# Kernel optimization log

Hardware: AMD Instinct MI355X
Metric: run time of the kernel (lower is better)

## Reference

```python
import jax, jax.numpy as jnp
import numpy as np

B, S, F, H = 8, 2048, 512, 4
W = 32            # local window size
DH = F // H       # head dim
EPS = 1e-5


def layer_norm(x, w, b):
    mu = jnp.mean(x, axis=-1, keepdims=True)
    var = jnp.var(x, axis=-1, keepdims=True)
    return (x - mu) * jax.lax.rsqrt(var + EPS) * w + b


def mha(x, w_in, b_in, w_out, b_out):
    # x: [..., L, F]; torch nn.MultiheadAttention self-attention (dropout inactive / eval)
    qkv = x @ w_in.T + b_in                      # [..., L, 3F]
    q, k, v = jnp.split(qkv, 3, axis=-1)
    lead = x.shape[:-2]
    L = x.shape[-2]

    def heads(t):  # [..., L, F] -> [..., H, L, DH]
        return jnp.swapaxes(t.reshape(*lead, L, H, DH), -3, -2)

    q, k, v = heads(q), heads(k), heads(v)
    scores = jnp.einsum('...hld,...hmd->...hlm', q, k) / np.sqrt(DH)
    p = jax.nn.softmax(scores, axis=-1)
    o = jnp.einsum('...hlm,...hmd->...hld', p, v)  # [..., H, L, DH]
    o = jnp.swapaxes(o, -3, -2).reshape(*lead, L, F)
    return o @ w_out.T + b_out


def setup_inputs() -> dict:
    key = jax.random.key(0)
    ks = jax.random.split(key, 16)
    s = 0.02
    p = lambda k, shape: jax.random.normal(k, shape, dtype=jnp.float32) * s
    return {
        'x': jax.random.normal(ks[0], (B, S, F), dtype=jnp.float32),
        'l_in_w': p(ks[1], (3 * F, F)), 'l_in_b': p(ks[2], (3 * F,)),
        'l_out_w': p(ks[3], (F, F)),   'l_out_b': p(ks[4], (F,)),
        'g_in_w': p(ks[5], (3 * F, F)), 'g_in_b': p(ks[6], (3 * F,)),
        'g_out_w': p(ks[7], (F, F)),   'g_out_b': p(ks[8], (F,)),
        'n1_w': jnp.ones((F,)), 'n1_b': jnp.zeros((F,)),
        'n2_w': jnp.ones((F,)), 'n2_b': jnp.zeros((F,)),
        'gate_w': p(ks[9], (F, 2 * F)), 'gate_b': p(ks[10], (F,)),
        'gln_w': jnp.ones((F,)), 'gln_b': jnp.zeros((F,)),
    }


def reference(x, l_in_w, l_in_b, l_out_w, l_out_b,
              g_in_w, g_in_b, g_out_w, g_out_b,
              n1_w, n1_b, n2_w, n2_b,
              gate_w, gate_b, gln_w, gln_b):
    # local branch: block-diagonal (windowed) self-attention, all windows batched
    xw = x.reshape(B, S // W, W, F)
    local = mha(xw, l_in_w, l_in_b, l_out_w, l_out_b).reshape(B, S, F)
    local = layer_norm(x + local, n1_w, n1_b)
    # global branch: full self-attention
    glob = mha(x, g_in_w, g_in_b, g_out_w, g_out_b)
    glob = layer_norm(x + glob, n2_w, n2_b)
    # learned gate fusion
    gi = jnp.concatenate([local, glob], axis=-1)
    gate = jax.nn.sigmoid(layer_norm(gi @ gate_w.T + gate_b, gln_w, gln_b))
    return gate * local + (1.0 - gate) * glob
```

## Files before the change

### kernel.cpp

```cpp
#include <hip/hip_runtime.h>
#include <stdint.h>

#define BB 8
#define SS 2048
#define FF 512
#define HH 4
#define TOK (BB * SS)

typedef unsigned short u16;
typedef short short8 __attribute__((ext_vector_type(8)));
typedef float f32x4 __attribute__((ext_vector_type(4)));
typedef float f32x16 __attribute__((ext_vector_type(16)));
typedef unsigned int u32x4 __attribute__((ext_vector_type(4)));

static __device__ __forceinline__ u16 f2bf(float f) {
  uint32_t u = __builtin_bit_cast(uint32_t, f);
  u = (u + 0x7fffu + ((u >> 16) & 1u)) >> 16;
  return (u16)u;
}

static __device__ __forceinline__ uint32_t cvtpk(float lo, float hi) {
  uint32_t r;
  asm("v_cvt_pk_bf16_f32 %0, %1, %2" : "=v"(r) : "v"(lo), "v"(hi));
  return r;
}

static __device__ __forceinline__ void cp16(void* lds, const void* g) {
  __builtin_amdgcn_global_load_lds(
      (const __attribute__((address_space(1))) void*)g,
      (__attribute__((address_space(3))) void*)lds, 16, 0, 0);
}

__global__ __launch_bounds__(256) void castk(const float* __restrict__ s,
                                             u16* __restrict__ d, int n) {
  const int i = (blockIdx.x * 256 + threadIdx.x) * 8;
  if (i >= n) return;
  float4 a = *(const float4*)(s + i);
  float4 b = *(const float4*)(s + i + 4);
  short8 o;
  o[0] = (short)f2bf(a.x); o[1] = (short)f2bf(a.y);
  o[2] = (short)f2bf(a.z); o[3] = (short)f2bf(a.w);
  o[4] = (short)f2bf(b.x); o[5] = (short)f2bf(b.y);
  o[6] = (short)f2bf(b.z); o[7] = (short)f2bf(b.w);
  *(short8*)(d + i) = o;
}

__global__ __launch_bounds__(256) void gemm_bt(
    const u16* __restrict__ A, const u16* __restrict__ B,
    const float* __restrict__ bias, float* __restrict__ Cf,
    u16* __restrict__ Cb, int M, int N, int K, int qcols, float qscale) {
  const int m0 = blockIdx.x << 7;
  const int n0 = blockIdx.y << 7;
  __shared__ u16 As[128 * 64];
  __shared__ u16 Bs[128 * 64];
  const int tid = threadIdx.x;
  const int wave = tid >> 6, lane = tid & 63;
  const int wr = wave >> 1, wc = wave & 1;

  f32x4 acc[4][4];
#pragma unroll
  for (int i = 0; i < 4; ++i)
#pragma unroll
    for (int j = 0; j < 4; ++j)
#pragma unroll
      for (int e = 0; e < 4; ++e) acc[i][j][e] = 0.f;

  for (int k0 = 0; k0 < K; k0 += 64) {
#pragma unroll
    for (int i = 0; i < 4; ++i) {
      const int base = (i * 4 + wave) << 10;
      const int lb = base + (lane << 4);
      const int r = lb >> 7;
      const int s = ((lb >> 4) & 7) ^ (r & 7);
      cp16((char*)As + base, A + (size_t)(m0 + r) * K + k0 + s * 8);
      cp16((char*)Bs + base, B + (size_t)(n0 + r) * K + k0 + s * 8);
    }
    __syncthreads();
#pragma unroll
    for (int kk = 0; kk < 2; ++kk) {
      short8 af[4], bfr[4];
#pragma unroll
      for (int mi = 0; mi < 4; ++mi) {
        const int r = wr * 64 + mi * 16 + (lane & 15);
        const int p = (kk * 4 + (lane >> 4)) ^ (r & 7);
        af[mi] = *(const short8*)(As + r * 64 + p * 8);
      }
#pragma unroll
      for (int ni = 0; ni < 4; ++ni) {
        const int r = wc * 64 + ni * 16 + (lane & 15);
        const int p = (kk * 4 + (lane >> 4)) ^ (r & 7);
        bfr[ni] = *(const short8*)(Bs + r * 64 + p * 8);
      }
#pragma unroll
      for (int mi = 0; mi < 4; ++mi)
#pragma unroll
        for (int ni = 0; ni < 4; ++ni)
          acc[mi][ni] = __builtin_amdgcn_mfma_f32_16x16x32_bf16(
              af[mi], bfr[ni], acc[mi][ni], 0, 0, 0);
    }
    __syncthreads();
  }
  const int rv = (lane >> 4) << 2;
  const int cn = lane & 15;
#pragma unroll
  for (int mi = 0; mi < 4; ++mi)
#pragma unroll
    for (int ni = 0; ni < 4; ++ni) {
      const int gn = n0 + wc * 64 + ni * 16 + cn;
      const float bv = bias ? bias[gn] : 0.f;
      const float sc = (gn < qcols) ? qscale : 1.f;
#pragma unroll
      for (int v = 0; v < 4; ++v) {
        const int gm = m0 + wr * 64 + mi * 16 + rv + v;
        const size_t off = (size_t)gm * N + gn;
        const float val = (acc[mi][ni][v] + bv) * sc;
        if (Cf) Cf[off] = val;
        if (Cb) Cb[off] = f2bf(val);
      }
    }
}

__global__ __launch_bounds__(256) void transpose_v(
    const u16* __restrict__ qkv, u16* __restrict__ vt) {
  const int bh = blockIdx.x, st = blockIdx.y, dt = blockIdx.z;
  const int b = bh >> 2, h = bh & 3;
  __shared__ u16 t[64][72];
  const int r = threadIdx.x >> 3;
  const int c8 = (threadIdx.x & 7) * 8;
#pragma unroll
  for (int ph = 0; ph < 2; ++ph) {
    const int srow = ph * 32 + r;
    const u16* src = qkv + (size_t)(b * SS + st * 64 + srow) * 1536 + 1024 +
                     h * 128 + dt * 64 + c8;
    *(short8*)&t[srow][c8] = *(const short8*)src;
  }
  __syncthreads();
#pragma unroll
  for (int ph = 0; ph < 2; ++ph) {
    const int drow = ph * 32 + r;
    short8 o;
#pragma unroll
    for (int j = 0; j < 8; ++j) o[j] = (short)t[c8 + j][drow];
    *(short8*)(vt + ((size_t)bh * 128 + dt * 64 + drow) * SS + st * 64 + c8) = o;
  }
}

template <typename GET>
static __device__ __forceinline__ short8 make_pa(int ks, GET get) {
  const int c0 = (2 * ks) & 3;
  u32x4 pw;
#pragma unroll
  for (int t = 0; t < 2; ++t) {
    uint32_t a = cvtpk(get(4 * c0 + 2 * t), get(4 * c0 + 2 * t + 1));
    uint32_t b = cvtpk(get(4 * (c0 + 1) + 2 * t), get(4 * (c0 + 1) + 2 * t + 1));
    auto r = __builtin_amdgcn_permlane32_swap(a, b, false, false);
    pw[t] = r[0];
    pw[2 + t] = r[1];
  }
  return __builtin_bit_cast(short8, pw);
}

__global__ __launch_bounds__(256) void attn_local(
    const u16* __restrict__ qkv, const u16* __restrict__ vt,
    u16* __restrict__ ao) {
  const int wave = threadIdx.x >> 6, lane = threadIdx.x & 63;
  const int u = blockIdx.x * 4 + wave;
  const int b = u >> 8, w = (u >> 2) & 63, h = u & 3;
  const int q = lane & 31, half = lane >> 5;

  const size_t qbase = (size_t)(b * SS + w * 32 + q) * 1536 + h * 128;
  short8 qf[8];
#pragma unroll
  for (int d8 = 0; d8 < 8; ++d8)
    qf[d8] = *(const short8*)(qkv + qbase + d8 * 16 + half * 8);

  f32x16 s;
#pragma unroll
  for (int e = 0; e < 16; ++e) s[e] = 0.f;
  const size_t kbase = qbase + 512;
#pragma unroll
  for (int d8 = 0; d8 < 8; ++d8) {
    short8 kf = *(const short8*)(qkv + kbase + d8 * 16 + half * 8);
    s = __builtin_amdgcn_mfma_f32_32x32x16_bf16(kf, qf[d8], s, 0, 0, 0);
  }
  float m = s[0];
#pragma unroll
  for (int e = 1; e < 16; ++e) m = fmaxf(m, s[e]);
  m = fmaxf(m, __shfl_xor(m, 32));
  float l = 0.f;
#pragma unroll
  for (int e = 0; e < 16; ++e) { s[e] = exp2f(s[e] - m); l += s[e]; }
  l += __shfl_xor(l, 32);

  f32x16 o[4];
#pragma unroll
  for (int nt = 0; nt < 4; ++nt)
#pragma unroll
    for (int e = 0; e < 16; ++e) o[nt][e] = 0.f;
  const size_t vbase = ((size_t)(b * 4 + h) * 128) * SS + w * 32;
#pragma unroll
  for (int ks = 0; ks < 2; ++ks) {
    short8 pa = make_pa(ks, [&](int e) { return s[e]; });
#pragma unroll
    for (int nt = 0; nt < 4; ++nt) {
      short8 vb = *(const short8*)(vt + vbase + (size_t)(nt * 32 + q) * SS +
                                   ks * 16 + half * 8);
      o[nt] = __builtin_amdgcn_mfma_f32_32x32x16_bf16(pa, vb, o[nt], 0, 0, 0);
    }
  }
  const float rl = 1.f / l;
  const size_t ob = (size_t)(b * SS + w * 32) * FF + h * 128;
#pragma unroll
  for (int e = 0; e < 16; ++e) {
    const int qr = (e & 3) + 8 * (e >> 2) + 4 * half;
    const float rf = __shfl(rl, qr);
#pragma unroll
    for (int nt = 0; nt < 4; ++nt)
      ao[ob + (size_t)qr * FF + nt * 32 + q] = f2bf(o[nt][e] * rf);
  }
}

__global__ __launch_bounds__(256) void attn_global(
    const u16* __restrict__ qkv, const u16* __restrict__ vt,
    u16* __restrict__ ao) {
  const int lb = (blockIdx.x & 7) * 64 + (blockIdx.x >> 3);
  const int bh = lb >> 4, qt = lb & 15;
  const int b = bh >> 2, h = bh & 3;
  const int wave = threadIdx.x >> 6, lane = threadIdx.x & 63;
  const int q = lane & 31, half = lane >> 5;

  __shared__ u16 Ks[2][64 * 128];
  __shared__ u16 Vs[2][128 * 64];

  short8 qf[8];
  const size_t qb = (size_t)(b * SS + qt * 128 + wave * 32 + q) * 1536 + h * 128;
#pragma unroll
  for (int d8 = 0; d8 < 8; ++d8)
    qf[d8] = *(const short8*)(qkv + qb + d8 * 16 + half * 8);

  f32x16 o[4];
#pragma unroll
  for (int nt = 0; nt < 4; ++nt)
#pragma unroll
    for (int e = 0; e < 16; ++e) o[nt][e] = 0.f;
  float m = -3e38f, lsum = 0.f;

  const size_t kbase = (size_t)b * SS * 1536 + 512 + h * 128;
  const size_t vbase = (size_t)bh * 128 * SS;

  auto STAGE = [&](int kt, int bsel) {
    u16* kd = Ks[bsel];
    u16* vd = Vs[bsel];
#pragma unroll
    for (int i = 0; i < 4; ++i) {
      const int base = (i * 4 + wave) << 10;
      const int lbk = base + (lane << 4);
      {
        const int r = lbk >> 8;
        const int sl = ((lbk >> 4) & 15) ^ (r & 7);
        cp16((char*)kd + base,
             qkv + kbase + (size_t)(kt * 64 + r) * 1536 + sl * 8);
      }
      {
        const int d = lbk >> 7;
        const int sl = ((lbk >> 4) & 7) ^ (d & 7);
        cp16((char*)vd + base, vt + vbase + (size_t)d * SS + kt * 64 + sl * 8);
      }
    }
  };
  STAGE(0, 0);
  __syncthreads();
  for (int kt = 0; kt < 32; ++kt) {
    const int cur = kt & 1;
    if (kt + 1 < 32) STAGE(kt + 1, cur ^ 1);
    const u16* Kb = Ks[cur];
    const u16* Vb = Vs[cur];

    f32x16 sa[2];
#pragma unroll
    for (int mt = 0; mt < 2; ++mt)
#pragma unroll
      for (int e = 0; e < 16; ++e) sa[mt][e] = 0.f;
#pragma unroll
    for (int mt = 0; mt < 2; ++mt) {
      const int kr = mt * 32 + q;
#pragma unroll
      for (int d8 = 0; d8 < 8; ++d8) {
        const int ps = (d8 * 2 + half) ^ (kr & 7);
        short8 kf = *(const short8*)(Kb + kr * 128 + ps * 8);
        sa[mt] = __builtin_amdgcn_mfma_f32_32x32x16_bf16(kf, qf[d8], sa[mt], 0, 0, 0);
      }
    }
    float pmax = sa[0][0];
#pragma unroll
    for (int e = 1; e < 16; ++e) pmax = fmaxf(pmax, sa[0][e]);
#pragma unroll
    for (int e = 0; e < 16; ++e) pmax = fmaxf(pmax, sa[1][e]);
    pmax = fmaxf(pmax, __shfl_xor(pmax, 32));
    if (__any(pmax > m + 8.f)) {
      const float mn = fmaxf(m, pmax);
      const float corr = exp2f(m - mn);
      m = mn;
      lsum *= corr;
#pragma unroll
      for (int e = 0; e < 16; ++e) {
        const float cf = __shfl(corr, (e & 3) + 8 * (e >> 2) + 4 * half);
#pragma unroll
        for (int nt = 0; nt < 4; ++nt) o[nt][e] *= cf;
      }
    }
    float la = 0.f;
#pragma unroll
    for (int mt = 0; mt < 2; ++mt)
#pragma unroll
      for (int e = 0; e < 16; ++e) {
        sa[mt][e] = exp2f(sa[mt][e] - m);
        la += sa[mt][e];
      }
    la += __shfl_xor(la, 32);
    lsum += la;
#pragma unroll
    for (int ks = 0; ks < 4; ++ks) {
      const int mt = ks >> 1;
      short8 pa = make_pa(ks, [&](int e) { return sa[mt][e]; });
#pragma unroll
      for (int nt = 0; nt < 4; ++nt) {
        const int d = nt * 32 + q;
        const int ps = (ks * 2 + half) ^ (d & 7);
        short8 vb = *(const short8*)(Vb + d * 64 + ps * 8);
        o[nt] = __builtin_amdgcn_mfma_f32_32x32x16_bf16(pa, vb, o[nt], 0, 0, 0);
      }
    }
    __syncthreads();
  }
  const float rl = 1.f / lsum;
  const size_t ob = (size_t)(b * SS + qt * 128 + wave * 32) * FF + h * 128;
#pragma unroll
  for (int e = 0; e < 16; ++e) {
    const int qr = (e & 3) + 8 * (e >> 2) + 4 * half;
    const float rf = __shfl(rl, qr);
#pragma unroll
    for (int nt = 0; nt < 4; ++nt)
      ao[ob + (size_t)qr * FF + nt * 32 + q] = f2bf(o[nt][e] * rf);
  }
}

__global__ __launch_bounds__(256) void resid_ln(
    float* __restrict__ y, const float* __restrict__ x,
    const float* __restrict__ w, const float* __restrict__ bv_,
    u16* __restrict__ lg) {
  const int wave = threadIdx.x >> 6, lane = threadIdx.x & 63;
  const size_t row = (size_t)blockIdx.x * 4 + wave;
  const int c = lane * 8;
  float* yr = y + row * FF;
  const float* xr = x + row * FF;
  float v[8];
  {
    float4 a0 = *(const float4*)(yr + c), a1 = *(const float4*)(yr + c + 4);
    float4 b0 = *(const float4*)(xr + c), b1 = *(const float4*)(xr + c + 4);
    v[0] = a0.x + b0.x; v[1] = a0.y + b0.y; v[2] = a0.z + b0.z; v[3] = a0.w + b0.w;
    v[4] = a1.x + b1.x; v[5] = a1.y + b1.y; v[6] = a1.z + b1.z; v[7] = a1.w + b1.w;
  }
  float s = 0.f, s2 = 0.f;
#pragma unroll
  for (int e = 0; e < 8; ++e) { s += v[e]; s2 += v[e] * v[e]; }
#pragma unroll
  for (int off = 1; off < 64; off <<= 1) {
    s += __shfl_xor(s, off);
    s2 += __shfl_xor(s2, off);
  }
  const float mu = s * (1.f / 512.f);
  const float var = s2 * (1.f / 512.f) - mu * mu;
  const float rs = rsqrtf(var + 1e-5f);
  float4 w0 = *(const float4*)(w + c), w1 = *(const float4*)(w + c + 4);
  float4 b0 = *(const float4*)(bv_ + c), b1 = *(const float4*)(bv_ + c + 4);
  const float wv[8] = {w0.x, w0.y, w0.z, w0.w, w1.x, w1.y, w1.z, w1.w};
  const float bb[8] = {b0.x, b0.y, b0.z, b0.w, b1.x, b1.y, b1.z, b1.w};
  short8 ob;
#pragma unroll
  for (int e = 0; e < 8; ++e) {
    v[e] = (v[e] - mu) * rs * wv[e] + bb[e];
    ob[e] = (short)f2bf(v[e]);
  }
  *(float4*)(yr + c) = make_float4(v[0], v[1], v[2], v[3]);
  *(float4*)(yr + c + 4) = make_float4(v[4], v[5], v[6], v[7]);
  *(short8*)(lg + row * 1024 + c) = ob;
}

__global__ __launch_bounds__(256) void gate_final(
    const float* __restrict__ gp, const float* __restrict__ loc,
    const float* __restrict__ glo, const float* __restrict__ w,
    const float* __restrict__ bv_, float* __restrict__ out) {
  const int wave = threadIdx.x >> 6, lane = threadIdx.x & 63;
  const size_t row = (size_t)blockIdx.x * 4 + wave;
  const int c = lane * 8;
  const float* gr = gp + row * FF;
  float v[8];
  {
    float4 a0 = *(const float4*)(gr + c), a1 = *(const float4*)(gr + c + 4);
    v[0] = a0.x; v[1] = a0.y; v[2] = a0.z; v[3] = a0.w;
    v[4] = a1.x; v[5] = a1.y; v[6] = a1.z; v[7] = a1.w;
  }
  float s = 0.f, s2 = 0.f;
#pragma unroll
  for (int e = 0; e < 8; ++e) { s += v[e]; s2 += v[e] * v[e]; }
#pragma unroll
  for (int off = 1; off < 64; off <<= 1) {
    s += __shfl_xor(s, off);
    s2 += __shfl_xor(s2, off);
  }
  const float mu = s * (1.f / 512.f);
  const float var = s2 * (1.f / 512.f) - mu * mu;
  const float rs = rsqrtf(var + 1e-5f);
  float4 w0 = *(const float4*)(w + c), w1 = *(const float4*)(w + c + 4);
  float4 b0 = *(const float4*)(bv_ + c), b1 = *(const float4*)(bv_ + c + 4);
  const float wv[8] = {w0.x, w0.y, w0.z, w0.w, w1.x, w1.y, w1.z, w1.w};
  const float bb[8] = {b0.x, b0.y, b0.z, b0.w, b1.x, b1.y, b1.z, b1.w};
  float4 l0 = *(const float4*)(loc + row * FF + c), l1 = *(const float4*)(loc + row * FF + c + 4);
  float4 g0 = *(const float4*)(glo + row * FF + c), g1 = *(const float4*)(glo + row * FF + c + 4);
  const float lv[8] = {l0.x, l0.y, l0.z, l0.w, l1.x, l1.y, l1.z, l1.w};
  const float gv[8] = {g0.x, g0.y, g0.z, g0.w, g1.x, g1.y, g1.z, g1.w};
  float r[8];
#pragma unroll
  for (int e = 0; e < 8; ++e) {
    const float z = (v[e] - mu) * rs * wv[e] + bb[e];
    const float gt = 1.f / (1.f + exp2f(-1.44269504f * z));
    r[e] = gt * lv[e] + (1.f - gt) * gv[e];
  }
  *(float4*)(out + row * FF + c) = make_float4(r[0], r[1], r[2], r[3]);
  *(float4*)(out + row * FF + c + 4) = make_float4(r[4], r[5], r[6], r[7]);
}

extern "C" void kernel_launch(void* const* d_in, const int* in_sizes, int n_in,
                              void* d_out, int out_size, void* d_ws,
                              size_t ws_size, hipStream_t stream) {
  const float* x       = (const float*)d_in[0];
  const float* l_in_w  = (const float*)d_in[1];
  const float* l_in_b  = (const float*)d_in[2];
  const float* l_out_w = (const float*)d_in[3];
  const float* l_out_b = (const float*)d_in[4];
  const float* g_in_w  = (const float*)d_in[5];
  const float* g_in_b  = (const float*)d_in[6];
  const float* g_out_w = (const float*)d_in[7];
  const float* g_out_b = (const float*)d_in[8];
  const float* n1_w    = (const float*)d_in[9];
  const float* n1_b    = (const float*)d_in[10];
  const float* n2_w    = (const float*)d_in[11];
  const float* n2_b    = (const float*)d_in[12];
  const float* gate_w  = (const float*)d_in[13];
  const float* gate_b  = (const float*)d_in[14];
  const float* gln_w   = (const float*)d_in[15];
  const float* gln_b   = (const float*)d_in[16];
  float* out = (float*)d_out;

  const float c1 = 0.12752724808f;

  char* ws = (char*)d_ws;
  u16* x_bf  = (u16*)(ws);
  u16* w_liw = (u16*)(ws + 16777216);
  u16* w_giw = (u16*)(ws + 18350080);
  u16* w_low = (u16*)(ws + 19922944);
  u16* w_gow = (u16*)(ws + 20447232);
  u16* w_gt  = (u16*)(ws + 20971520);
  u16* qkv   = (u16*)(ws + 22020096);
  u16* vt    = (u16*)(ws + 72351744);
  u16* ato   = (u16*)(ws + 89128960);
  float* locf = (float*)(ws + 105906176);
  float* glof = (float*)(ws + 139460608);
  u16* lgbf  = (u16*)(ws + 173015040);
  float* gpre = (float*)(ws + 22020096);

  castk<<<4096, 256, 0, stream>>>(x, x_bf, 8388608);
  castk<<<384, 256, 0, stream>>>(l_in_w, w_liw, 786432);
  castk<<<384, 256, 0, stream>>>(g_in_w, w_giw, 786432);
  castk<<<128, 256, 0, stream>>>(l_out_w, w_low, 262144);
  castk<<<128, 256, 0, stream>>>(g_out_w, w_gow, 262144);
  castk<<<256, 256, 0, stream>>>(gate_w, w_gt, 524288);

  gemm_bt<<<dim3(128, 12), 256, 0, stream>>>(x_bf, w_liw, l_in_b, nullptr, qkv,
                                             TOK, 1536, 512, 512, c1);
  transpose_v<<<dim3(32, 32, 2), 256, 0, stream>>>(qkv, vt);
  attn_local<<<512, 256, 0, stream>>>(qkv, vt, ato);
  gemm_bt<<<dim3(128, 4), 256, 0, stream>>>(ato, w_low, l_out_b, locf, nullptr,
                                            TOK, 512, 512, 0, 1.f);
  resid_ln<<<4096, 256, 0, stream>>>(locf, x, n1_w, n1_b, lgbf);

  gemm_bt<<<dim3(128, 12), 256, 0, stream>>>(x_bf, w_giw, g_in_b, nullptr, qkv,
                                             TOK, 1536, 512, 512, c1);
  transpose_v<<<dim3(32, 32, 2), 256, 0, stream>>>(qkv, vt);
  attn_global<<<512, 256, 0, stream>>>(qkv, vt, ato);
  gemm_bt<<<dim3(128, 4), 256, 0, stream>>>(ato, w_gow, g_out_b, glof, nullptr,
                                            TOK, 512, 512, 0, 1.f);
  resid_ln<<<4096, 256, 0, stream>>>(glof, x, n2_w, n2_b, lgbf + 512);

  gemm_bt<<<dim3(128, 4), 256, 0, stream>>>(lgbf, w_gt, gate_b, gpre, nullptr,
                                            TOK, 512, 1024, 0, 1.f);
  gate_final<<<4096, 256, 0, stream>>>(gpre, locf, glof, gln_w, gln_b, out);
}
```

Baseline: 471.6 us.

## Load K/V fragments directly from global memory in global attention, dropping LDS staging

The global attention kernel no longer double-buffers K and V tiles through shared memory with async copies and barriers. Each wave now reads its K and V MFMA operands straight from global memory (relying on L1/L2 caching) through running pointers, and the launch bounds ask for two blocks per CU. The row max and row sum reductions become tree reductions to shorten dependency chains. This removes LDS traffic and per-tile barriers, but every wave in a block now fetches the same K/V data separately and exposes global load latency without explicit prefetch.

```diff
diff --git a/kernel.cpp b/kernel.cpp
--- a/kernel.cpp
+++ b/kernel.cpp
@@ -220,8 +220,8 @@
   }
 }
 
-__global__ __launch_bounds__(256) void attn_global(
-    const u16* __restrict__ qkv, const u16* __restrict__ vt,
+__global__ __launch_bounds__(256, 2) void attn_global(
+    const u16* __restrict__ qkv, const u16* __restrict__ vtp,
     u16* __restrict__ ao) {
   const int lb = (blockIdx.x & 7) * 64 + (blockIdx.x >> 3);
   const int bh = lb >> 4, qt = lb & 15;
@@ -229,9 +229,6 @@
   const int wave = threadIdx.x >> 6, lane = threadIdx.x & 63;
   const int q = lane & 31, half = lane >> 5;
 
-  __shared__ u16 Ks[2][64 * 128];
-  __shared__ u16 Vs[2][128 * 64];
-
   short8 qf[8];
   const size_t qb = (size_t)(b * SS + qt * 128 + wave * 32 + q) * 1536 + h * 128;
 #pragma unroll
@@ -245,58 +242,40 @@
     for (int e = 0; e < 16; ++e) o[nt][e] = 0.f;
   float m = -3e38f, lsum = 0.f;
 
-  const size_t kbase = (size_t)b * SS * 1536 + 512 + h * 128;
-  const size_t vbase = (size_t)bh * 128 * SS;
-
-  auto STAGE = [&](int kt, int bsel) {
-    u16* kd = Ks[bsel];
-    u16* vd = Vs[bsel];
-#pragma unroll
-    for (int i = 0; i < 4; ++i) {
-      const int base = (i * 4 + wave) << 10;
-      const int lbk = base + (lane << 4);
-      {
-        const int r = lbk >> 8;
-        const int sl = ((lbk >> 4) & 15) ^ (r & 7);
-        cp16((char*)kd + base,
-             qkv + kbase + (size_t)(kt * 64 + r) * 1536 + sl * 8);
-      }
-      {
-        const int d = lbk >> 7;
-        const int sl = ((lbk >> 4) & 7) ^ (d & 7);
-        cp16((char*)vd + base, vt + vbase + (size_t)d * SS + kt * 64 + sl * 8);
-      }
-    }
-  };
-  STAGE(0, 0);
-  __syncthreads();
+  const u16* pk0 = qkv + (size_t)b * SS * 1536 + 512 + (size_t)h * 128 +
+                   (size_t)q * 1536 + half * 8;
+  const u16* pk1 = pk0 + (size_t)32 * 1536;
+  const u16* pvb = vtp + (size_t)bh * 128 * SS + (size_t)q * SS + half * 8;
+  const u16* pv0 = pvb;
+  const u16* pv1 = pvb + (size_t)32 * SS;
+  const u16* pv2 = pvb + (size_t)64 * SS;
+  const u16* pv3 = pvb + (size_t)96 * SS;
+
   for (int kt = 0; kt < 32; ++kt) {
-    const int cur = kt & 1;
-    if (kt + 1 < 32) STAGE(kt + 1, cur ^ 1);
-    const u16* Kb = Ks[cur];
-    const u16* Vb = Vs[cur];
-
     f32x16 sa[2];
 #pragma unroll
     for (int mt = 0; mt < 2; ++mt)
 #pragma unroll
       for (int e = 0; e < 16; ++e) sa[mt][e] = 0.f;
 #pragma unroll
-    for (int mt = 0; mt < 2; ++mt) {
-      const int kr = mt * 32 + q;
-#pragma unroll
-      for (int d8 = 0; d8 < 8; ++d8) {
-        const int ps = (d8 * 2 + half) ^ (kr & 7);
-        short8 kf = *(const short8*)(Kb + kr * 128 + ps * 8);
-        sa[mt] = __builtin_amdgcn_mfma_f32_32x32x16_bf16(kf, qf[d8], sa[mt], 0, 0, 0);
-      }
-    }
-    float pmax = sa[0][0];
-#pragma unroll
-    for (int e = 1; e < 16; ++e) pmax = fmaxf(pmax, sa[0][e]);
-#pragma unroll
-    for (int e = 0; e < 16; ++e) pmax = fmaxf(pmax, sa[1][e]);
-    pmax = fmaxf(pmax, __shfl_xor(pmax, 32));
+    for (int d8 = 0; d8 < 8; ++d8) {
+      short8 kf0 = *(const short8*)(pk0 + d8 * 16);
+      sa[0] = __builtin_amdgcn_mfma_f32_32x32x16_bf16(kf0, qf[d8], sa[0], 0, 0, 0);
+    }
+#pragma unroll
+    for (int d8 = 0; d8 < 8; ++d8) {
+      short8 kf1 = *(const short8*)(pk1 + d8 * 16);
+      sa[1] = __builtin_amdgcn_mfma_f32_32x32x16_bf16(kf1, qf[d8], sa[1], 0, 0, 0);
+    }
+    float t[16];
+#pragma unroll
+    for (int e = 0; e < 16; ++e) t[e] = fmaxf(sa[0][e], sa[1][e]);
+#pragma unroll
+    for (int st = 8; st >= 1; st >>= 1)
+#pragma unroll
+      for (int e = 0; e < 8; ++e)
+        if (e < st) t[e] = fmaxf(t[e], t[e + st]);
+    float pmax = fmaxf(t[0], __shfl_xor(t[0], 32));
     if (__any(pmax > m + 8.f)) {
       const float mn = fmaxf(m, pmax);
       const float corr = exp2f(m - mn);
@@ -309,29 +288,35 @@
         for (int nt = 0; nt < 4; ++nt) o[nt][e] *= cf;
       }
     }
-    float la = 0.f;
 #pragma unroll
     for (int mt = 0; mt < 2; ++mt)
 #pragma unroll
-      for (int e = 0; e < 16; ++e) {
-        sa[mt][e] = exp2f(sa[mt][e] - m);
-        la += sa[mt][e];
-      }
-    la += __shfl_xor(la, 32);
-    lsum += la;
+      for (int e = 0; e < 16; ++e) sa[mt][e] = exp2f(sa[mt][e] - m);
+    float u[16];
+#pragma unroll
+    for (int e = 0; e < 16; ++e) u[e] = sa[0][e] + sa[1][e];
+#pragma unroll
+    for (int st = 8; st >= 1; st >>= 1)
+#pragma unroll
+      for (int e = 0; e < 8; ++e)
+        if (e < st) u[e] += u[e + st];
+    lsum += u[0] + __shfl_xor(u[0], 32);
 #pragma unroll
     for (int ks = 0; ks < 4; ++ks) {
       const int mt = ks >> 1;
       short8 pa = make_pa(ks, [&](int e) { return sa[mt][e]; });
-#pragma unroll
-      for (int nt = 0; nt < 4; ++nt) {
-        const int d = nt * 32 + q;
-        const int ps = (ks * 2 + half) ^ (d & 7);
-        short8 vb = *(const short8*)(Vb + d * 64 + ps * 8);
-        o[nt] = __builtin_amdgcn_mfma_f32_32x32x16_bf16(pa, vb, o[nt], 0, 0, 0);
-      }
-    }
-    __syncthreads();
+      short8 vb0 = *(const short8*)(pv0 + ks * 16);
+      short8 vb1 = *(const short8*)(pv1 + ks * 16);
+      short8 vb2 = *(const short8*)(pv2 + ks * 16);
+      short8 vb3 = *(const short8*)(pv3 + ks * 16);
+      o[0] = __builtin_amdgcn_mfma_f32_32x32x16_bf16(pa, vb0, o[0], 0, 0, 0);
+      o[1] = __builtin_amdgcn_mfma_f32_32x32x16_bf16(pa, vb1, o[1], 0, 0, 0);
+      o[2] = __builtin_amdgcn_mfma_f32_32x32x16_bf16(pa, vb2, o[2], 0, 0, 0);
+      o[3] = __builtin_amdgcn_mfma_f32_32x32x16_bf16(pa, vb3, o[3], 0, 0, 0);
+    }
+    pk0 += (size_t)64 * 1536;
+    pk1 += (size_t)64 * 1536;
+    pv0 += 64; pv1 += 64; pv2 += 64; pv3 += 64;
   }
   const float rl = 1.f / lsum;
   const size_t ob = (size_t)(b * SS + qt * 128 + wave * 32) * FF + h * 128;
```

Measured after the change: 580.5 us. 1.23x slower.

## Store projection outputs in bf16, reuse bf16 LN results, tree-reduce softmax stats

Applied to the files above, without the earlier changes.

The output projections now write bf16 instead of fp32, and resid_ln no longer writes back an fp32 normalized tensor. gate_final reads the local and global branches from the bf16 concat buffer instead of separate fp32 arrays, which cuts memory traffic in several elementwise kernels. The global attention loop also raises wave priority around the MFMA blocks and replaces the serial max and sum chains with tree reductions to shorten dependency latency. The cost is extra bf16 rounding of the projection output before the residual and of the final gating operands, which lowers accuracy.

```diff
diff --git a/kernel.cpp b/kernel.cpp
--- a/kernel.cpp
+++ b/kernel.cpp
@@ -17,6 +17,9 @@
   uint32_t u = __builtin_bit_cast(uint32_t, f);
   u = (u + 0x7fffu + ((u >> 16) & 1u)) >> 16;
   return (u16)u;
+}
+static __device__ __forceinline__ float bf2f(u16 u) {
+  return __builtin_bit_cast(float, (uint32_t)u << 16);
 }
 
 static __device__ __forceinline__ uint32_t cvtpk(float lo, float hi) {
@@ -281,6 +284,7 @@
     for (int mt = 0; mt < 2; ++mt)
 #pragma unroll
       for (int e = 0; e < 16; ++e) sa[mt][e] = 0.f;
+    __builtin_amdgcn_s_setprio(1);
 #pragma unroll
     for (int mt = 0; mt < 2; ++mt) {
       const int kr = mt * 32 + q;
@@ -291,12 +295,16 @@
         sa[mt] = __builtin_amdgcn_mfma_f32_32x32x16_bf16(kf, qf[d8], sa[mt], 0, 0, 0);
       }
     }
-    float pmax = sa[0][0];
-#pragma unroll
-    for (int e = 1; e < 16; ++e) pmax = fmaxf(pmax, sa[0][e]);
-#pragma unroll
-    for (int e = 0; e < 16; ++e) pmax = fmaxf(pmax, sa[1][e]);
-    pmax = fmaxf(pmax, __shfl_xor(pmax, 32));
+    __builtin_amdgcn_s_setprio(0);
+    float t[16];
+#pragma unroll
+    for (int e = 0; e < 16; ++e) t[e] = fmaxf(sa[0][e], sa[1][e]);
+#pragma unroll
+    for (int st = 8; st >= 1; st >>= 1)
+#pragma unroll
+      for (int e = 0; e < 8; ++e)
+        if (e < st) t[e] = fmaxf(t[e], t[e + st]);
+    float pmax = fmaxf(t[0], __shfl_xor(t[0], 32));
     if (__any(pmax > m + 8.f)) {
       const float mn = fmaxf(m, pmax);
       const float corr = exp2f(m - mn);
@@ -309,16 +317,20 @@
         for (int nt = 0; nt < 4; ++nt) o[nt][e] *= cf;
       }
     }
-    float la = 0.f;
 #pragma unroll
     for (int mt = 0; mt < 2; ++mt)
 #pragma unroll
-      for (int e = 0; e < 16; ++e) {
-        sa[mt][e] = exp2f(sa[mt][e] - m);
-        la += sa[mt][e];
-      }
-    la += __shfl_xor(la, 32);
-    lsum += la;
+      for (int e = 0; e < 16; ++e) sa[mt][e] = exp2f(sa[mt][e] - m);
+    float u[16];
+#pragma unroll
+    for (int e = 0; e < 16; ++e) u[e] = sa[0][e] + sa[1][e];
+#pragma unroll
+    for (int st = 8; st >= 1; st >>= 1)
+#pragma unroll
+      for (int e = 0; e < 8; ++e)
+        if (e < st) u[e] += u[e + st];
+    lsum += u[0] + __shfl_xor(u[0], 32);
+    __builtin_amdgcn_s_setprio(1);
 #pragma unroll
     for (int ks = 0; ks < 4; ++ks) {
       const int mt = ks >> 1;
@@ -331,6 +343,7 @@
         o[nt] = __builtin_amdgcn_mfma_f32_32x32x16_bf16(pa, vb, o[nt], 0, 0, 0);
       }
     }
+    __builtin_amdgcn_s_setprio(0);
     __syncthreads();
   }
   const float rl = 1.f / lsum;
@@ -346,20 +359,22 @@
 }
 
 __global__ __launch_bounds__(256) void resid_ln(
-    float* __restrict__ y, const float* __restrict__ x,
+    const u16* __restrict__ yb, const float* __restrict__ x,
     const float* __restrict__ w, const float* __restrict__ bv_,
     u16* __restrict__ lg) {
   const int wave = threadIdx.x >> 6, lane = threadIdx.x & 63;
   const size_t row = (size_t)blockIdx.x * 4 + wave;
   const int c = lane * 8;
-  float* yr = y + row * FF;
+  const u16* yr = yb + row * FF;
   const float* xr = x + row * FF;
   float v[8];
   {
-    float4 a0 = *(const float4*)(yr + c), a1 = *(const float4*)(yr + c + 4);
+    short8 a = *(const short8*)(yr + c);
     float4 b0 = *(const float4*)(xr + c), b1 = *(const float4*)(xr + c + 4);
-    v[0] = a0.x + b0.x; v[1] = a0.y + b0.y; v[2] = a0.z + b0.z; v[3] = a0.w + b0.w;
-    v[4] = a1.x + b1.x; v[5] = a1.y + b1.y; v[6] = a1.z + b1.z; v[7] = a1.w + b1.w;
+    v[0] = bf2f((u16)a[0]) + b0.x; v[1] = bf2f((u16)a[1]) + b0.y;
+    v[2] = bf2f((u16)a[2]) + b0.z; v[3] = bf2f((u16)a[3]) + b0.w;
+    v[4] = bf2f((u16)a[4]) + b1.x; v[5] = bf2f((u16)a[5]) + b1.y;
+    v[6] = bf2f((u16)a[6]) + b1.z; v[7] = bf2f((u16)a[7]) + b1.w;
   }
   float s = 0.f, s2 = 0.f;
 #pragma unroll
@@ -378,19 +393,15 @@
   const float bb[8] = {b0.x, b0.y, b0.z, b0.w, b1.x, b1.y, b1.z, b1.w};
   short8 ob;
 #pragma unroll
-  for (int e = 0; e < 8; ++e) {
-    v[e] = (v[e] - mu) * rs * wv[e] + bb[e];
-    ob[e] = (short)f2bf(v[e]);
-  }
-  *(float4*)(yr + c) = make_float4(v[0], v[1], v[2], v[3]);
-  *(float4*)(yr + c + 4) = make_float4(v[4], v[5], v[6], v[7]);
+  for (int e = 0; e < 8; ++e)
+    ob[e] = (short)f2bf((v[e] - mu) * rs * wv[e] + bb[e]);
   *(short8*)(lg + row * 1024 + c) = ob;
 }
 
 __global__ __launch_bounds__(256) void gate_final(
-    const float* __restrict__ gp, const float* __restrict__ loc,
-    const float* __restrict__ glo, const float* __restrict__ w,
-    const float* __restrict__ bv_, float* __restrict__ out) {
+    const float* __restrict__ gp, const u16* __restrict__ lg,
+    const float* __restrict__ w, const float* __restrict__ bv_,
+    float* __restrict__ out) {
   const int wave = threadIdx.x >> 6, lane = threadIdx.x & 63;
   const size_t row = (size_t)blockIdx.x * 4 + wave;
   const int c = lane * 8;
@@ -416,16 +427,14 @@
   float4 b0 = *(const float4*)(bv_ + c), b1 = *(const float4*)(bv_ + c + 4);
   const float wv[8] = {w0.x, w0.y, w0.z, w0.w, w1.x, w1.y, w1.z, w1.w};
   const float bb[8] = {b0.x, b0.y, b0.z, b0.w, b1.x, b1.y, b1.z, b1.w};
-  float4 l0 = *(const float4*)(loc + row * FF + c), l1 = *(const float4*)(loc + row * FF + c + 4);
-  float4 g0 = *(const float4*)(glo + row * FF + c), g1 = *(const float4*)(glo + row * FF + c + 4);
-  const float lv[8] = {l0.x, l0.y, l0.z, l0.w, l1.x, l1.y, l1.z, l1.w};
-  const float gv[8] = {g0.x, g0.y, g0.z, g0.w, g1.x, g1.y, g1.z, g1.w};
+  short8 l8 = *(const short8*)(lg + row * 1024 + c);
+  short8 g8 = *(const short8*)(lg + row * 1024 + 512 + c);
   float r[8];
 #pragma unroll
   for (int e = 0; e < 8; ++e) {
     const float z = (v[e] - mu) * rs * wv[e] + bb[e];
     const float gt = 1.f / (1.f + exp2f(-1.44269504f * z));
-    r[e] = gt * lv[e] + (1.f - gt) * gv[e];
+    r[e] = gt * bf2f((u16)l8[e]) + (1.f - gt) * bf2f((u16)g8[e]);
   }
   *(float4*)(out + row * FF + c) = make_float4(r[0], r[1], r[2], r[3]);
   *(float4*)(out + row * FF + c + 4) = make_float4(r[4], r[5], r[6], r[7]);
@@ -465,9 +474,8 @@
   u16* qkv   = (u16*)(ws + 22020096);
   u16* vt    = (u16*)(ws + 72351744);
   u16* ato   = (u16*)(ws + 89128960);
-  float* locf = (float*)(ws + 105906176);
-  float* glof = (float*)(ws + 139460608);
-  u16* lgbf  = (u16*)(ws + 173015040);
+  u16* prj   = (u16*)(ws + 105906176);
+  u16* lgbf  = (u16*)(ws + 122683392);
   float* gpre = (float*)(ws + 22020096);
 
   castk<<<4096, 256, 0, stream>>>(x, x_bf, 8388608);
@@ -481,19 +489,19 @@
                                              TOK, 1536, 512, 512, c1);
   transpose_v<<<dim3(32, 32, 2), 256, 0, stream>>>(qkv, vt);
   attn_local<<<512, 256, 0, stream>>>(qkv, vt, ato);
-  gemm_bt<<<dim3(128, 4), 256, 0, stream>>>(ato, w_low, l_out_b, locf, nullptr,
+  gemm_bt<<<dim3(128, 4), 256, 0, stream>>>(ato, w_low, l_out_b, nullptr, prj,
                                             TOK, 512, 512, 0, 1.f);
-  resid_ln<<<4096, 256, 0, stream>>>(locf, x, n1_w, n1_b, lgbf);
+  resid_ln<<<4096, 256, 0, stream>>>(prj, x, n1_w, n1_b, lgbf);
 
   gemm_bt<<<dim3(128, 12), 256, 0, stream>>>(x_bf, w_giw, g_in_b, nullptr, qkv,
                                              TOK, 1536, 512, 512, c1);
   transpose_v<<<dim3(32, 32, 2), 256, 0, stream>>>(qkv, vt);
   attn_global<<<512, 256, 0, stream>>>(qkv, vt, ato);
-  gemm_bt<<<dim3(128, 4), 256, 0, stream>>>(ato, w_gow, g_out_b, glof, nullptr,
+  gemm_bt<<<dim3(128, 4), 256, 0, stream>>>(ato, w_gow, g_out_b, nullptr, prj,
                                             TOK, 512, 512, 0, 1.f);
-  resid_ln<<<4096, 256, 0, stream>>>(glof, x, n2_w, n2_b, lgbf + 512);
+  resid_ln<<<4096, 256, 0, stream>>>(prj, x, n2_w, n2_b, lgbf + 512);
 
   gemm_bt<<<dim3(128, 4), 256, 0, stream>>>(lgbf, w_gt, gate_b, gpre, nullptr,
                                             TOK, 512, 1024, 0, 1.f);
-  gate_final<<<4096, 256, 0, stream>>>(gpre, locf, glof, gln_w, gln_b, out);
-}
+  gate_final<<<4096, 256, 0, stream>>>(gpre, lgbf, gln_w, gln_b, out);
+}
```

Result: no change. 466.7 us (-1.0%).
